# Kernel tuning notes

Hardware: AMD Instinct MI355X
Metric: run time of the kernel (lower is better)

## Reference

```python
import jax, jax.numpy as jnp
import numpy as np
import math

VOCAB = 50257
BLOCK = 2048
NE = 768


def setup_inputs() -> dict:
    key = jax.random.key(0)
    ks = jax.random.split(key, 12)
    s = 0.02
    idx = jax.random.randint(ks[0], (4, 2048), 0, VOCAB, dtype=jnp.int64 if jax.config.jax_enable_x64 else jnp.int32)
    tok_emb = jax.random.normal(ks[1], (VOCAB, NE), jnp.float32) * s
    pos_emb = jax.random.normal(ks[2], (BLOCK, NE), jnp.float32) * s
    Wk = jax.random.normal(ks[3], (NE, NE), jnp.float32) * s
    bk = jnp.zeros((NE,), jnp.float32)
    Wq = jax.random.normal(ks[4], (NE, NE), jnp.float32) * s
    bq = jnp.zeros((NE,), jnp.float32)
    Wv = jax.random.normal(ks[5], (NE, NE), jnp.float32) * s
    bv = jnp.zeros((NE,), jnp.float32)
    ln_g = jnp.ones((NE,), jnp.float32)
    ln_b = jnp.zeros((NE,), jnp.float32)
    Wh = jax.random.normal(ks[6], (NE, VOCAB), jnp.float32) * s
    bh = jnp.zeros((VOCAB,), jnp.float32)
    return {"idx": idx, "tok_emb": tok_emb, "pos_emb": pos_emb, "Wq": Wq, "bq": bq,
            "Wk": Wk, "bk": bk, "Wv": Wv, "bv": bv, "ln_g": ln_g, "ln_b": ln_b,
            "Wh": Wh, "bh": bh}


def reference(idx, tok_emb, pos_emb, Wq, bq, Wk, bk, Wv, bv, ln_g, ln_b, Wh, bh):
    B, T = idx.shape
    C = tok_emb.shape[1]
    x = tok_emb[idx] + pos_emb[:T]  # [B,T,C]
    q = jnp.einsum('btc,cd->btd', x, Wq) + bq
    k = jnp.einsum('btc,cd->btd', x, Wk) + bk
    v = jnp.einsum('btc,cd->btd', x, Wv) + bv
    att = jnp.einsum('btd,bsd->bts', q, k) / math.sqrt(C)  # [B,T,T]
    causal = jnp.tril(jnp.ones((T, T), bool))
    att = jnp.where(causal, att, -jnp.inf)
    att = jax.nn.softmax(att, axis=-1)
    y = jnp.einsum('bts,bsd->btd', att, v)
    # LayerNorm (eps=1e-5, torch default)
    mu = jnp.mean(y, axis=-1, keepdims=True)
    var = jnp.mean((y - mu) ** 2, axis=-1, keepdims=True)
    yn = (y - mu) * jax.lax.rsqrt(var + 1e-5) * ln_g + ln_b
    logits = jnp.einsum('btc,cv->btv', yn, Wh) + bh
    return logits
```

## Files before the change

kernel.cpp:

```cpp
#include <hip/hip_runtime.h>
#include <hip/hip_bf16.h>
#include <math.h>

typedef __bf16 bf16x8 __attribute__((ext_vector_type(8)));
typedef float  f32x4  __attribute__((ext_vector_type(4)));

#define GAS(p) ((const __attribute__((address_space(1))) void*)(p))
#define LAS(p) ((__attribute__((address_space(3))) void*)(p))

static constexpr int NE = 768;

__global__ __launch_bounds__(256) void k_embed(const int* __restrict__ idx,
    const float* __restrict__ tok, const float* __restrict__ pos,
    __hip_bfloat16* __restrict__ xb)
{
    int bt = blockIdx.x;
    int t  = bt & 2047;
    int token = idx[bt];
    const float* te = tok + (size_t)token * NE;
    const float* pe = pos + (size_t)t * NE;
    __hip_bfloat16* o = xb + (size_t)bt * NE;
    for (int c = threadIdx.x; c < NE; c += 256)
        o[c] = __float2bfloat16(te[c] + pe[c]);
}

__global__ __launch_bounds__(256) void k_transpose_f32_bf16(
    const float* __restrict__ in, __hip_bfloat16* __restrict__ out,
    int R, int C, int outRows)
{
    __shared__ float tile[32][33];
    int c0 = blockIdx.x * 32, r0 = blockIdx.y * 32;
    int tx = threadIdx.x & 31, ty = threadIdx.x >> 5;
    #pragma unroll
    for (int i = 0; i < 32; i += 8) {
        int r = r0 + ty + i, c = c0 + tx;
        tile[ty + i][tx] = (r < R && c < C) ? in[(size_t)r * C + c] : 0.f;
    }
    __syncthreads();
    #pragma unroll
    for (int i = 0; i < 32; i += 8) {
        int oc = c0 + ty + i, orr = r0 + tx;
        if (oc < outRows && orr < R)
            out[(size_t)oc * R + orr] = __float2bfloat16(tile[tx][ty + i]);
    }
}

__global__ __launch_bounds__(256) void k_transpose_bf16(
    const __hip_bfloat16* __restrict__ in, __hip_bfloat16* __restrict__ out,
    int R, int C)
{
    __shared__ __hip_bfloat16 tile[32][33];
    size_t boff = (size_t)blockIdx.z * R * C;
    int c0 = blockIdx.x * 32, r0 = blockIdx.y * 32;
    int tx = threadIdx.x & 31, ty = threadIdx.x >> 5;
    #pragma unroll
    for (int i = 0; i < 32; i += 8)
        tile[ty + i][tx] = in[boff + (size_t)(r0 + ty + i) * C + (c0 + tx)];
    __syncthreads();
    #pragma unroll
    for (int i = 0; i < 32; i += 8)
        out[boff + (size_t)(c0 + ty + i) * R + (r0 + tx)] = tile[tx][ty + i];
}

__global__ __launch_bounds__(256) void k_pack_bias(const float* __restrict__ bq,
    const float* __restrict__ bk, const float* __restrict__ bv, float* __restrict__ o)
{
    int i = blockIdx.x * 256 + threadIdx.x;
    if (i < 768) o[i] = bq[i];
    else if (i < 1536) o[i] = bk[i - 768];
    else if (i < 2304) o[i] = bv[i - 1536];
}

template<int MODE>
__global__ __launch_bounds__(256) void k_gemm(
    const __hip_bfloat16* __restrict__ A, const __hip_bfloat16* __restrict__ Bt,
    int K, int lda, int ldb,
    size_t strideA, size_t strideB, size_t strideC,
    float* __restrict__ outf, int ldc, int ncols,
    const float* __restrict__ bias, float scale,
    __hip_bfloat16* __restrict__ oq, __hip_bfloat16* __restrict__ ok,
    __hip_bfloat16* __restrict__ ov)
{
    int bn = blockIdx.x, bm = blockIdx.y, bz = blockIdx.z;
    if (MODE == 1 && bn > bm) return;
    __shared__ __align__(16) __hip_bfloat16 As[128 * 32];
    __shared__ __align__(16) __hip_bfloat16 Bs[128 * 32];
    const __hip_bfloat16* Ab = A  + bz * strideA + (size_t)bm * 128 * lda;
    const __hip_bfloat16* Bb = Bt + bz * strideB + (size_t)bn * 128 * ldb;
    int tid = threadIdx.x, w = tid >> 6, lane = tid & 63;
    int wr = w >> 1, wc = w & 1;
    f32x4 acc[4][4] = {};
    int sr = tid >> 2, sc = (tid & 3) * 8;
    int lr = lane & 15, lk = (lane >> 4) * 8;

    for (int k0 = 0; k0 < K; k0 += 32) {
        __syncthreads();
        #pragma unroll
        for (int i = 0; i < 2; ++i) {
            __builtin_amdgcn_global_load_lds(GAS(Ab + (size_t)(i * 64 + sr) * lda + k0 + sc),
                                             LAS((char*)As + i * 4096 + w * 1024), 16, 0, 0);
            __builtin_amdgcn_global_load_lds(GAS(Bb + (size_t)(i * 64 + sr) * ldb + k0 + sc),
                                             LAS((char*)Bs + i * 4096 + w * 1024), 16, 0, 0);
        }
        __syncthreads();
        bf16x8 af[4], bfv[4];
        #pragma unroll
        for (int mi = 0; mi < 4; ++mi)
            af[mi] = *(const bf16x8*)(As + (wr * 64 + mi * 16 + lr) * 32 + lk);
        #pragma unroll
        for (int ni = 0; ni < 4; ++ni)
            bfv[ni] = *(const bf16x8*)(Bs + (wc * 64 + ni * 16 + lr) * 32 + lk);
        #pragma unroll
        for (int mi = 0; mi < 4; ++mi)
            #pragma unroll
            for (int ni = 0; ni < 4; ++ni)
                acc[mi][ni] = __builtin_amdgcn_mfma_f32_16x16x32_bf16(af[mi], bfv[ni], acc[mi][ni], 0, 0, 0);
    }

    int r4 = (lane >> 4) * 4;
    #pragma unroll
    for (int mi = 0; mi < 4; ++mi) {
        #pragma unroll
        for (int ni = 0; ni < 4; ++ni) {
            #pragma unroll
            for (int r = 0; r < 4; ++r) {
                int row = bm * 128 + wr * 64 + mi * 16 + r4 + r;
                int col = bn * 128 + wc * 64 + ni * 16 + lr;
                float v = acc[mi][ni][r];
                if constexpr (MODE == 0) {
                    v += bias[col];
                    __hip_bfloat16 h = __float2bfloat16(v);
                    if (col < 768)       oq[(size_t)row * 768 + col]          = h;
                    else if (col < 1536) ok[(size_t)row * 768 + (col - 768)]  = h;
                    else                 ov[(size_t)row * 768 + (col - 1536)] = h;
                } else if constexpr (MODE == 1) {
                    outf[bz * strideC + (size_t)row * ldc + col] = v * scale;
                } else {
                    outf[bz * strideC + (size_t)row * ldc + col] = v;
                }
            }
        }
    }
}

__global__ __launch_bounds__(512, 2) void k_gemm_head(
    const __hip_bfloat16* __restrict__ A,
    const __hip_bfloat16* __restrict__ Bt,
    float* __restrict__ out, const float* __restrict__ bias, int ldc, int ncols)
{
    constexpr int K = 768, NT = K / 64;
    __shared__ __align__(16) __hip_bfloat16 As[2][256 * 64];
    __shared__ __align__(16) __hip_bfloat16 Bs[2][256 * 64];

    const int bn = blockIdx.x, bm = blockIdx.y;
    const int tid = threadIdx.x;
    const int w = tid >> 6, lane = tid & 63;
    const int wr = w >> 2, wc = w & 3;
    const int lr = lane & 15, lu = lane >> 4;
    const int rswz = lr & 7;

    const int srow = tid >> 3;
    const int sunit = (tid & 7) ^ (srow & 7);
    const size_t Abase = (size_t)bm * 256 * K;
    const size_t Bbase = (size_t)bn * 256 * K;

    auto stageA = [&](int kt, int c, int p) {
        const __hip_bfloat16* src = A + Abase + (size_t)(c * 64 + srow) * K + kt * 64 + sunit * 8;
        __builtin_amdgcn_global_load_lds(GAS(src), LAS(&As[p][c * 4096 + tid * 8]), 16, 0, 0);
    };
    auto stageB = [&](int kt, int c, int p) {
        const __hip_bfloat16* src = Bt + Bbase + (size_t)(c * 64 + srow) * K + kt * 64 + sunit * 8;
        __builtin_amdgcn_global_load_lds(GAS(src), LAS(&Bs[p][c * 4096 + tid * 8]), 16, 0, 0);
    };
    auto rdA = [&](int p, int m, int kk) {
        return *(const bf16x8*)&As[p][(wr * 128 + m * 16 + lr) * 64 + ((kk * 4 + lu) ^ rswz) * 8];
    };
    auto rdB = [&](int p, int n, int kk) {
        return *(const bf16x8*)&Bs[p][(wc * 64 + n * 16 + lr) * 64 + ((kk * 4 + lu) ^ rswz) * 8];
    };

    f32x4 acc[8][4] = {};

    stageB(0, 0, 0); stageB(0, 1, 0); stageB(0, 2, 0); stageB(0, 3, 0);
    stageA(0, 0, 0); stageA(0, 1, 0); stageA(0, 2, 0); stageA(0, 3, 0);
    stageB(1, 0, 1); stageB(1, 1, 1); stageB(1, 2, 1); stageB(1, 3, 1);
    stageA(1, 0, 1); stageA(1, 2, 1);

#define QUAD(Q)                                                                                          \
    {   bf16x8 a00 = rdA(p, 2*(Q),     0), a01 = rdA(p, 2*(Q),     1);                                   \
        bf16x8 a10 = rdA(p, 2*(Q) + 1, 0), a11 = rdA(p, 2*(Q) + 1, 1);                                   \
        __builtin_amdgcn_s_setprio(1);                                                                   \
        _Pragma("unroll")                                                                                \
        for (int n = 0; n < 4; ++n) {                                                                    \
            acc[2*(Q)][n]     = __builtin_amdgcn_mfma_f32_16x16x32_bf16(a00, bf[n][0], acc[2*(Q)][n],     0, 0, 0); \
            acc[2*(Q)][n]     = __builtin_amdgcn_mfma_f32_16x16x32_bf16(a01, bf[n][1], acc[2*(Q)][n],     0, 0, 0); \
            acc[2*(Q) + 1][n] = __builtin_amdgcn_mfma_f32_16x16x32_bf16(a10, bf[n][0], acc[2*(Q) + 1][n], 0, 0, 0); \
            acc[2*(Q) + 1][n] = __builtin_amdgcn_mfma_f32_16x16x32_bf16(a11, bf[n][1], acc[2*(Q) + 1][n], 0, 0, 0); \
        }                                                                                                \
        __builtin_amdgcn_s_setprio(0); }

    for (int kt = 0; kt < NT; ++kt) {
        const int p = kt & 1, pn = p ^ 1;
        if (kt + 1 < NT) {
            stageA(kt + 1, 1, pn); stageA(kt + 1, 3, pn);
            asm volatile("s_waitcnt vmcnt(8)" ::: "memory");
        } else {
            asm volatile("s_waitcnt vmcnt(0)" ::: "memory");
        }
        asm volatile("s_barrier" ::: "memory");
        bf16x8 bf[4][2];
        #pragma unroll
        for (int n = 0; n < 4; ++n) { bf[n][0] = rdB(p, n, 0); bf[n][1] = rdB(p, n, 1); }
        QUAD(0)
        asm volatile("s_barrier" ::: "memory");
        if (kt + 2 < NT) { stageB(kt + 2, 0, p); stageB(kt + 2, 1, p); }
        QUAD(1)
        asm volatile("s_barrier" ::: "memory");
        if (kt + 2 < NT) { stageB(kt + 2, 2, p); stageB(kt + 2, 3, p); }
        QUAD(2)
        asm volatile("s_barrier" ::: "memory");
        if (kt + 2 < NT) { stageA(kt + 2, 0, p); stageA(kt + 2, 2, p); }
        QUAD(3)
        asm volatile("s_barrier" ::: "memory");
    }
#undef QUAD

    const int r4 = lu * 4;
    #pragma unroll
    for (int m = 0; m < 8; ++m) {
        #pragma unroll
        for (int n = 0; n < 4; ++n) {
            int col = bn * 256 + wc * 64 + n * 16 + lr;
            if (col < ncols) {
                float bv_ = bias[col];
                #pragma unroll
                for (int r = 0; r < 4; ++r) {
                    int row = bm * 256 + wr * 128 + m * 16 + r4 + r;
                    out[(size_t)row * ldc + col] = acc[m][n][r] + bv_;
                }
            }
        }
    }
}

__global__ __launch_bounds__(256) void k_softmax(const float* __restrict__ att,
    __hip_bfloat16* __restrict__ P, int T)
{
    int t = blockIdx.x, b = blockIdx.y;
    const float* row = att + ((size_t)b * T + t) * T;
    __hip_bfloat16* prow = P + ((size_t)b * T + t) * T;
    int n = t + 1;
    __shared__ float red[256];
    float mx = -1e30f;
    for (int s = threadIdx.x; s < n; s += 256) mx = fmaxf(mx, row[s]);
    red[threadIdx.x] = mx; __syncthreads();
    for (int o = 128; o > 0; o >>= 1) {
        if (threadIdx.x < o) red[threadIdx.x] = fmaxf(red[threadIdx.x], red[threadIdx.x + o]);
        __syncthreads();
    }
    mx = red[0]; __syncthreads();
    float sum = 0.f;
    for (int s = threadIdx.x; s < n; s += 256) sum += expf(row[s] - mx);
    red[threadIdx.x] = sum; __syncthreads();
    for (int o = 128; o > 0; o >>= 1) {
        if (threadIdx.x < o) red[threadIdx.x] += red[threadIdx.x + o];
        __syncthreads();
    }
    float inv = 1.f / red[0];
    for (int s = threadIdx.x; s < T; s += 256)
        prow[s] = __float2bfloat16(s < n ? expf(row[s] - mx) * inv : 0.f);
}

__global__ __launch_bounds__(256) void k_layernorm(const float* __restrict__ y,
    const float* __restrict__ g, const float* __restrict__ b,
    __hip_bfloat16* __restrict__ yn)
{
    int row = blockIdx.x;
    const float* yr = y + (size_t)row * NE;
    float s = 0.f, s2 = 0.f;
    for (int c = threadIdx.x; c < NE; c += 256) { float v = yr[c]; s += v; s2 += v * v; }
    __shared__ float r1[256], r2[256];
    r1[threadIdx.x] = s; r2[threadIdx.x] = s2; __syncthreads();
    for (int o = 128; o > 0; o >>= 1) {
        if (threadIdx.x < o) { r1[threadIdx.x] += r1[threadIdx.x + o]; r2[threadIdx.x] += r2[threadIdx.x + o]; }
        __syncthreads();
    }
    float mu = r1[0] / NE;
    float var = r2[0] / NE - mu * mu;
    float rs = rsqrtf(var + 1e-5f);
    __hip_bfloat16* o = yn + (size_t)row * NE;
    for (int c = threadIdx.x; c < NE; c += 256)
        o[c] = __float2bfloat16((yr[c] - mu) * rs * g[c] + b[c]);
}

extern "C" void kernel_launch(void* const* d_in, const int* in_sizes, int n_in,
                              void* d_out, int out_size, void* d_ws, size_t ws_size,
                              hipStream_t stream)
{
    const int*   idx  = (const int*)  d_in[0];
    const float* tok  = (const float*)d_in[1];
    const float* pos  = (const float*)d_in[2];
    const float* Wq   = (const float*)d_in[3];
    const float* bq   = (const float*)d_in[4];
    const float* Wk   = (const float*)d_in[5];
    const float* bk   = (const float*)d_in[6];
    const float* Wv   = (const float*)d_in[7];
    const float* bv   = (const float*)d_in[8];
    const float* ln_g = (const float*)d_in[9];
    const float* ln_b = (const float*)d_in[10];
    const float* Wh   = (const float*)d_in[11];
    const float* bh   = (const float*)d_in[12];
    float* out = (float*)d_out;

    const int B = 4, T = 2048, C = 768, V = 50257, Vp = 50432;

    char* p = (char*)d_ws;
    auto take = [&](size_t bytes) { char* r = p; p += (bytes + 255) & ~(size_t)255; return r; };
    __hip_bfloat16* xb    = (__hip_bfloat16*)take((size_t)B * T * C * 2);
    __hip_bfloat16* wqkvT = (__hip_bfloat16*)take((size_t)3 * C * C * 2);
    float*          bqkv  = (float*)take((size_t)3 * C * 4);
    __hip_bfloat16* qb    = (__hip_bfloat16*)take((size_t)B * T * C * 2);
    __hip_bfloat16* kb    = (__hip_bfloat16*)take((size_t)B * T * C * 2);
    __hip_bfloat16* vb    = (__hip_bfloat16*)take((size_t)B * T * C * 2);
    __hip_bfloat16* vT    = (__hip_bfloat16*)take((size_t)B * T * C * 2);
    float*          att   = (float*)take((size_t)B * T * T * 4);
    __hip_bfloat16* P     = (__hip_bfloat16*)take((size_t)B * T * T * 2);
    float*          y     = (float*)take((size_t)B * T * C * 4);
    __hip_bfloat16* yn    = (__hip_bfloat16*)take((size_t)B * T * C * 2);
    __hip_bfloat16* whT   = (__hip_bfloat16*)att;

    float scale = 1.0f / sqrtf((float)C);

    k_embed<<<dim3(B * T), 256, 0, stream>>>(idx, tok, pos, xb);
    k_transpose_f32_bf16<<<dim3(24, 24), 256, 0, stream>>>(Wq, wqkvT,             C, C, C);
    k_transpose_f32_bf16<<<dim3(24, 24), 256, 0, stream>>>(Wk, wqkvT + C * C,     C, C, C);
    k_transpose_f32_bf16<<<dim3(24, 24), 256, 0, stream>>>(Wv, wqkvT + 2 * C * C, C, C, C);
    k_pack_bias<<<dim3(9), 256, 0, stream>>>(bq, bk, bv, bqkv);

    k_gemm<0><<<dim3(18, 64, 1), 256, 0, stream>>>(xb, wqkvT, C, C, C, 0, 0, 0,
        nullptr, 0, 0, bqkv, 1.f, qb, kb, vb);

    k_transpose_bf16<<<dim3(24, 64, B), 256, 0, stream>>>(vb, vT, T, C);

    k_gemm<1><<<dim3(16, 16, B), 256, 0, stream>>>(qb, kb, C, C, C,
        (size_t)T * C, (size_t)T * C, (size_t)T * T, att, T, 0, nullptr, scale,
        nullptr, nullptr, nullptr);

    k_softmax<<<dim3(T, B), 256, 0, stream>>>(att, P, T);

    k_gemm<2><<<dim3(6, 16, B), 256, 0, stream>>>(P, vT, T, T, T,
        (size_t)T * T, (size_t)C * T, (size_t)T * C, y, C, 0, nullptr, 1.f,
        nullptr, nullptr, nullptr);

    k_transpose_f32_bf16<<<dim3(Vp / 32, 24), 256, 0, stream>>>(Wh, whT, C, V, Vp);

    k_layernorm<<<dim3(B * T), 256, 0, stream>>>(y, ln_g, ln_b, yn);

    k_gemm_head<<<dim3(Vp / 256, 32), 512, 0, stream>>>(yn, whT, out, bh, V, V);
}
```

Before: 1.367 ms.

## Skip masked K-tiles in PV GEMM, remap head grid for XCDs, vectorize softmax

The PV GEMM (MODE 2) now stops its K loop at the causal diagonal and schedules the heaviest row blocks first by reversing bm. The LM-head GEMM remaps blockIdx.x so that contiguous column tiles land on the same XCD, which should improve L2 reuse. Softmax loads each row once into registers with float4 reads, keeps the exponentials, uses the fast __expf, and writes probabilities only up to the next 128-aligned boundary, skipping the zeros beyond it. In exchange, softmax now assumes T is exactly 2048, and P beyond the boundary is left unwritten, which relies on the GEMM never reading it.

```diff
diff --git a/kernel.cpp b/kernel.cpp
--- a/kernel.cpp
+++ b/kernel.cpp
@@ -82,6 +82,7 @@
     __hip_bfloat16* __restrict__ ov)
 {
     int bn = blockIdx.x, bm = blockIdx.y, bz = blockIdx.z;
+    if constexpr (MODE == 2) bm = (int)gridDim.y - 1 - bm;
     if (MODE == 1 && bn > bm) return;
     __shared__ __align__(16) __hip_bfloat16 As[128 * 32];
     __shared__ __align__(16) __hip_bfloat16 Bs[128 * 32];
@@ -93,7 +94,9 @@
     int sr = tid >> 2, sc = (tid & 3) * 8;
     int lr = lane & 15, lk = (lane >> 4) * 8;
 
-    for (int k0 = 0; k0 < K; k0 += 32) {
+    const int kend = (MODE == 2) ? (bm + 1) * 128 : K;
+
+    for (int k0 = 0; k0 < kend; k0 += 32) {
         __syncthreads();
         #pragma unroll
         for (int i = 0; i < 2; ++i) {
@@ -152,7 +155,11 @@
     __shared__ __align__(16) __hip_bfloat16 As[2][256 * 64];
     __shared__ __align__(16) __hip_bfloat16 Bs[2][256 * 64];
 
-    const int bn = blockIdx.x, bm = blockIdx.y;
+    const int Nx = (int)gridDim.x;
+    const int qq = Nx >> 3, rr = Nx & 7;
+    const int xcd = (int)blockIdx.x & 7, xidx = (int)blockIdx.x >> 3;
+    const int bn = (xcd < rr ? xcd * (qq + 1) : rr * (qq + 1) + (xcd - rr) * qq) + xidx;
+    const int bm = blockIdx.y;
     const int tid = threadIdx.x;
     const int w = tid >> 6, lane = tid & 63;
     const int wr = w >> 2, wc = w & 3;
@@ -249,26 +256,51 @@
     int t = blockIdx.x, b = blockIdx.y;
     const float* row = att + ((size_t)b * T + t) * T;
     __hip_bfloat16* prow = P + ((size_t)b * T + t) * T;
-    int n = t + 1;
+    const int n = t + 1;
+    const int nz = ((t >> 7) + 1) << 7;
     __shared__ float red[256];
+    float4 v[2];
     float mx = -1e30f;
-    for (int s = threadIdx.x; s < n; s += 256) mx = fmaxf(mx, row[s]);
+    #pragma unroll
+    for (int j = 0; j < 2; ++j) {
+        int e = (threadIdx.x + j * 256) * 4;
+        v[j] = *(const float4*)(row + e);
+        #pragma unroll
+        for (int k = 0; k < 4; ++k)
+            if (e + k < n) mx = fmaxf(mx, ((const float*)&v[j])[k]);
+    }
     red[threadIdx.x] = mx; __syncthreads();
     for (int o = 128; o > 0; o >>= 1) {
         if (threadIdx.x < o) red[threadIdx.x] = fmaxf(red[threadIdx.x], red[threadIdx.x + o]);
         __syncthreads();
     }
     mx = red[0]; __syncthreads();
+    float ev[8];
     float sum = 0.f;
-    for (int s = threadIdx.x; s < n; s += 256) sum += expf(row[s] - mx);
+    #pragma unroll
+    for (int j = 0; j < 2; ++j) {
+        int e = (threadIdx.x + j * 256) * 4;
+        #pragma unroll
+        for (int k = 0; k < 4; ++k) {
+            float x = ((const float*)&v[j])[k];
+            float ex = (e + k < n) ? __expf(x - mx) : 0.f;
+            ev[j * 4 + k] = ex;
+            sum += ex;
+        }
+    }
     red[threadIdx.x] = sum; __syncthreads();
     for (int o = 128; o > 0; o >>= 1) {
         if (threadIdx.x < o) red[threadIdx.x] += red[threadIdx.x + o];
         __syncthreads();
     }
     float inv = 1.f / red[0];
-    for (int s = threadIdx.x; s < T; s += 256)
-        prow[s] = __float2bfloat16(s < n ? expf(row[s] - mx) * inv : 0.f);
+    #pragma unroll
+    for (int j = 0; j < 2; ++j) {
+        int e = (threadIdx.x + j * 256) * 4;
+        #pragma unroll
+        for (int k = 0; k < 4; ++k)
+            if (e + k < nz) prow[e + k] = __float2bfloat16(ev[j * 4 + k] * inv);
+    }
 }
 
 __global__ __launch_bounds__(256) void k_layernorm(const float* __restrict__ y,
```

After: 1.274 ms. -6.8%, faster.
